# Optimization experiments

Hardware: AMD Instinct MI355X
Metric: run time of the kernel (lower is better)

Reference implementation:

```python
import jax, jax.numpy as jnp
import numpy as np

D_MODEL = 1024
N_HEADS = 16
DEPTH = D_MODEL // N_HEADS
D_FF = 4096
B, S = 2, 2048
EPS = 1e-5


def _layernorm(x, g, b):
    mu = jnp.mean(x, axis=-1, keepdims=True)
    var = jnp.mean(jnp.square(x - mu), axis=-1, keepdims=True)
    return (x - mu) * jax.lax.rsqrt(var + EPS) * g + b


def setup_inputs() -> dict:
    key = jax.random.key(0)
    ks = jax.random.split(key, 16)
    sd = 0.02
    d = {
        'x': jax.random.normal(ks[0], (B, S, D_MODEL), dtype=jnp.float32),
        'mask': jnp.ones((B, S), dtype=jnp.int32),
        'wq_w': jax.random.normal(ks[1], (D_MODEL, D_MODEL), dtype=jnp.float32) * sd,
        'wq_b': jnp.zeros((D_MODEL,), dtype=jnp.float32),
        'wk_w': jax.random.normal(ks[2], (D_MODEL, D_MODEL), dtype=jnp.float32) * sd,
        'wk_b': jnp.zeros((D_MODEL,), dtype=jnp.float32),
        'wv_w': jax.random.normal(ks[3], (D_MODEL, D_MODEL), dtype=jnp.float32) * sd,
        'wv_b': jnp.zeros((D_MODEL,), dtype=jnp.float32),
        'wo_w': jax.random.normal(ks[4], (D_MODEL, D_MODEL), dtype=jnp.float32) * sd,
        'wo_b': jnp.zeros((D_MODEL,), dtype=jnp.float32),
        'ffn_w1': jax.random.normal(ks[5], (D_MODEL, D_FF), dtype=jnp.float32) * sd,
        'ffn_b1': jnp.zeros((D_FF,), dtype=jnp.float32),
        'ffn_w2': jax.random.normal(ks[6], (D_FF, D_MODEL), dtype=jnp.float32) * sd,
        'ffn_b2': jnp.zeros((D_MODEL,), dtype=jnp.float32),
        'ln1_g': jnp.ones((D_MODEL,), dtype=jnp.float32),
        'ln1_b': jnp.zeros((D_MODEL,), dtype=jnp.float32),
        'ln2_g': jnp.ones((D_MODEL,), dtype=jnp.float32),
        'ln2_b': jnp.zeros((D_MODEL,), dtype=jnp.float32),
    }
    return d


def reference(x, mask, wq_w, wq_b, wk_w, wk_b, wv_w, wv_b, wo_w, wo_b,
              ffn_w1, ffn_b1, ffn_w2, ffn_b2, ln1_g, ln1_b, ln2_g, ln2_b):
    b, s, _ = x.shape
    # projections [B,S,D] -> [B,H,S,depth]
    def split_heads(t):
        return t.reshape(b, s, N_HEADS, DEPTH).transpose(0, 2, 1, 3)
    q = split_heads(x @ wq_w + wq_b)
    k = split_heads(x @ wk_w + wk_b)
    v = split_heads(x @ wv_w + wv_b)
    # scores [B,H,S,S]
    logits = jnp.einsum('bhqd,bhkd->bhqk', q, k) / jnp.sqrt(jnp.float32(DEPTH))
    m = mask[:, None, None, :]  # [B,1,1,S] broadcast over heads/query
    logits = jnp.where(m == 0, jnp.float32(-1e9), logits)
    attn = jax.nn.softmax(logits, axis=-1)
    ctx = jnp.einsum('bhqk,bhkd->bhqd', attn, v)
    ctx = ctx.transpose(0, 2, 1, 3).reshape(b, s, D_MODEL)
    attn_out = ctx @ wo_w + wo_b
    out1 = _layernorm(x + attn_out, ln1_g, ln1_b)
    ffn = jax.nn.relu(out1 @ ffn_w1 + ffn_b1) @ ffn_w2 + ffn_b2
    out2 = _layernorm(out1 + ffn, ln2_g, ln2_b)
    return out2
```

## Files before the change

### kernel.cpp

```cpp
#include <hip/hip_runtime.h>
#include <hip/hip_bf16.h>

#define D_MODEL 1024
#define N_HEADS 16
#define DEPTH   64
#define D_FF    4096
#define BATCH   2
#define SEQ     2048
#define NTOK    (BATCH * SEQ)
#define EPS     1e-5f

typedef __attribute__((ext_vector_type(8))) short short8;
typedef __attribute__((ext_vector_type(4))) float f32x4;
typedef __attribute__((ext_vector_type(4))) unsigned short ushort4v;
typedef __attribute__((ext_vector_type(8))) unsigned short ushort8v;

__device__ __forceinline__ unsigned short f2bf(float f) {
    union { __hip_bfloat16 h; unsigned short u; } cv;
    cv.h = __float2bfloat16(f);
    return cv.u;
}

__device__ __forceinline__ void gload16(const unsigned short* g, unsigned short* lds) {
    __builtin_amdgcn_global_load_lds(
        (const __attribute__((address_space(1))) void*)g,
        (__attribute__((address_space(3))) void*)lds, 16, 0, 0);
}

__global__ __launch_bounds__(256) void cast_bf16_kernel(
    const float* __restrict__ in, unsigned short* __restrict__ out, int n)
{
    int i = (blockIdx.x * 256 + threadIdx.x) * 8;
    if (i >= n) return;
    f32x4 a = *(const f32x4*)&in[i];
    f32x4 b = *(const f32x4*)&in[i + 4];
    ushort8v o;
    o[0] = f2bf(a[0]); o[1] = f2bf(a[1]); o[2] = f2bf(a[2]); o[3] = f2bf(a[3]);
    o[4] = f2bf(b[0]); o[5] = f2bf(b[1]); o[6] = f2bf(b[2]); o[7] = f2bf(b[3]);
    *(ushort8v*)&out[i] = o;
}

__global__ __launch_bounds__(256) void transpose_cast_kernel(
    const float* __restrict__ W, unsigned short* __restrict__ WT, int K, int N)
{
    __shared__ float t[64][65];
    const int bk = blockIdx.y * 64, bn = blockIdx.x * 64;
    const int c4 = threadIdx.x & 15, r0 = threadIdx.x >> 4;
#pragma unroll
    for (int i = 0; i < 4; ++i) {
        int k = r0 + i * 16;
        f32x4 v = *(const f32x4*)&W[(size_t)(bk + k) * N + bn + c4 * 4];
#pragma unroll
        for (int jj = 0; jj < 4; ++jj) t[k][c4 * 4 + jj] = v[jj];
    }
    __syncthreads();
#pragma unroll
    for (int i = 0; i < 4; ++i) {
        int n = r0 + i * 16;
        ushort4v o;
#pragma unroll
        for (int jj = 0; jj < 4; ++jj) o[jj] = f2bf(t[c4 * 4 + jj][n]);
        *(ushort4v*)&WT[(size_t)(bn + n) * K + bk + c4 * 4] = o;
    }
}

__global__ __launch_bounds__(256) void concat3_kernel(
    const float* __restrict__ a, const float* __restrict__ b,
    const float* __restrict__ c, float* __restrict__ o)
{
    int i = blockIdx.x * 256 + threadIdx.x;
    if (i < 1024) o[i] = a[i];
    else if (i < 2048) o[i] = b[i - 1024];
    else if (i < 3072) o[i] = c[i - 2048];
}

__global__ __launch_bounds__(256) void vtrans_kernel(
    const unsigned short* __restrict__ QKV, unsigned short* __restrict__ Vt)
{
    __shared__ unsigned short T[64][72];
    const int st = blockIdx.x * 64;
    const int h = blockIdx.y, b = blockIdx.z;
    const int tid = threadIdx.x;
    const size_t tok0 = (size_t)b * SEQ;
    const int LD = 3 * D_MODEL;
    const int r = tid >> 3, c8 = (tid & 7) * 8;
#pragma unroll
    for (int p = 0; p < 2; ++p) {
        int row = p * 32 + r;
        *(ushort8v*)&T[row][c8] =
            *(const ushort8v*)&QKV[(tok0 + st + row) * LD + 2048 + h * 64 + c8];
    }
    __syncthreads();
    const int bh = b * N_HEADS + h;
#pragma unroll
    for (int p = 0; p < 2; ++p) {
        int d = p * 32 + r;
        ushort8v o;
#pragma unroll
        for (int e = 0; e < 8; ++e) o[e] = T[c8 + e][d];
        *(ushort8v*)&Vt[((size_t)bh * 64 + d) * SEQ + st + c8] = o;
    }
}

__global__ __launch_bounds__(512, 2) void gemm256_kernel(
    const unsigned short* __restrict__ A, const unsigned short* __restrict__ BT,
    const float* __restrict__ bias, float* __restrict__ C,
    unsigned short* __restrict__ Cb,
    int M, int N, int lda, int kLen, int ksplit, int relu, int out_bf)
{
    __shared__ unsigned short As[2][256 * 64];
    __shared__ unsigned short Bs[2][256 * 64];
    const int tid = threadIdx.x;
    const int lane = tid & 63, w = tid >> 6;
    const int wr = w >> 2, wc = w & 3;
    const int lr = lane & 15, g = lane >> 4;

    const int nwg = gridDim.x;
    int wg = blockIdx.x;
    if ((nwg & 7) == 0) wg = (wg & 7) * (nwg >> 3) + (wg >> 3);
    if (ksplit > 1) {
        const int ntile = nwg / ksplit;
        const int split = wg / ntile;
        wg = wg % ntile;
        A  += (size_t)split * kLen;
        BT += (size_t)split * kLen;
        C  += (size_t)split * M * N;
    }
    const int gx = N >> 8;
    const int bm = (wg / gx) * 256, bn = (wg % gx) * 256;

    const int srow = (w << 3) + (lane >> 3);
    const int scol = ((lane & 7) ^ (lane >> 3)) << 3;
    const int ldst = (w << 9);

#define STG(P, Xs, bufi, hf, rb, k0)                                            \
    {                                                                            \
        gload16(P + (size_t)((rb) + (hf) * 128 + srow) * lda + (k0) + scol,      \
                &Xs[bufi][(hf) * 8192 + ldst]);                                  \
        gload16(P + (size_t)((rb) + (hf) * 128 + 64 + srow) * lda + (k0) + scol, \
                &Xs[bufi][(hf) * 8192 + 4096 + ldst]);                           \
    }

    const int NS = kLen >> 6;
    f32x4 acc[8][4] = {};

    STG(A,  As, 0, 0, bm, 0); STG(A,  As, 0, 1, bm, 0);
    STG(BT, Bs, 0, 0, bn, 0); STG(BT, Bs, 0, 1, bn, 0);
    if (NS > 1) { STG(BT, Bs, 1, 0, bn, 64); STG(BT, Bs, 1, 1, bn, 64); }
    asm volatile("s_waitcnt vmcnt(4)" ::: "memory");
    __builtin_amdgcn_s_barrier();
    asm volatile("" ::: "memory");

    int buf = 0;
    short8 af[4][2], b0[2][2], b1[2][2];
    for (int s = 0; s < NS; ++s) {
        const int kn1 = (s + 1) << 6, kn2 = (s + 2) << 6;

#pragma unroll
        for (int i = 0; i < 4; ++i)
#pragma unroll
            for (int kk = 0; kk < 2; ++kk)
                af[i][kk] = *(const short8*)&As[buf][(wr * 128 + i * 16 + lr) * 64
                                                    + (((kk * 4 + g) ^ (lr & 7)) << 3)];
#pragma unroll
        for (int j = 0; j < 2; ++j)
#pragma unroll
            for (int kk = 0; kk < 2; ++kk)
                b0[j][kk] = *(const short8*)&Bs[buf][(wc * 64 + j * 16 + lr) * 64
                                                    + (((kk * 4 + g) ^ (lr & 7)) << 3)];
        if (s + 1 < NS) STG(A, As, buf ^ 1, 0, bm, kn1);
        asm volatile("" ::: "memory");
        __builtin_amdgcn_s_barrier();
        asm volatile("" ::: "memory");
        __builtin_amdgcn_s_setprio(1);
#pragma unroll
        for (int i = 0; i < 4; ++i)
#pragma unroll
            for (int j = 0; j < 2; ++j) {
                acc[i][j] = __builtin_amdgcn_mfma_f32_16x16x32_bf16(af[i][0], b0[j][0], acc[i][j], 0, 0, 0);
                acc[i][j] = __builtin_amdgcn_mfma_f32_16x16x32_bf16(af[i][1], b0[j][1], acc[i][j], 0, 0, 0);
            }
        __builtin_amdgcn_s_setprio(0);
        asm volatile("" ::: "memory");
        __builtin_amdgcn_s_barrier();
        asm volatile("" ::: "memory");

#pragma unroll
        for (int j = 0; j < 2; ++j)
#pragma unroll
            for (int kk = 0; kk < 2; ++kk)
                b1[j][kk] = *(const short8*)&Bs[buf][(wc * 64 + (j + 2) * 16 + lr) * 64
                                                    + (((kk * 4 + g) ^ (lr & 7)) << 3)];
        if (s + 1 < NS) STG(A, As, buf ^ 1, 1, bm, kn1);
        asm volatile("" ::: "memory");
        __builtin_amdgcn_s_barrier();
        asm volatile("" ::: "memory");
        __builtin_amdgcn_s_setprio(1);
#pragma unroll
        for (int i = 0; i < 4; ++i)
#pragma unroll
            for (int j = 0; j < 2; ++j) {
                acc[i][j + 2] = __builtin_amdgcn_mfma_f32_16x16x32_bf16(af[i][0], b1[j][0], acc[i][j + 2], 0, 0, 0);
                acc[i][j + 2] = __builtin_amdgcn_mfma_f32_16x16x32_bf16(af[i][1], b1[j][1], acc[i][j + 2], 0, 0, 0);
            }
        __builtin_amdgcn_s_setprio(0);
        asm volatile("" ::: "memory");
        __builtin_amdgcn_s_barrier();
        asm volatile("" ::: "memory");

#pragma unroll
        for (int i = 0; i < 4; ++i)
#pragma unroll
            for (int kk = 0; kk < 2; ++kk)
                af[i][kk] = *(const short8*)&As[buf][(wr * 128 + 64 + i * 16 + lr) * 64
                                                    + (((kk * 4 + g) ^ (lr & 7)) << 3)];
        if (s + 2 < NS) STG(BT, Bs, buf, 0, bn, kn2);
        asm volatile("" ::: "memory");
        __builtin_amdgcn_s_barrier();
        asm volatile("" ::: "memory");
        __builtin_amdgcn_s_setprio(1);
#pragma unroll
        for (int i = 0; i < 4; ++i)
#pragma unroll
            for (int j = 0; j < 2; ++j) {
                acc[i + 4][j] = __builtin_amdgcn_mfma_f32_16x16x32_bf16(af[i][0], b0[j][0], acc[i + 4][j], 0, 0, 0);
                acc[i + 4][j] = __builtin_amdgcn_mfma_f32_16x16x32_bf16(af[i][1], b0[j][1], acc[i + 4][j], 0, 0, 0);
            }
        __builtin_amdgcn_s_setprio(0);
        asm volatile("" ::: "memory");
        __builtin_amdgcn_s_barrier();
        asm volatile("" ::: "memory");

        if (s + 2 < NS) STG(BT, Bs, buf, 1, bn, kn2);
        asm volatile("" ::: "memory");
        __builtin_amdgcn_s_barrier();
        asm volatile("" ::: "memory");
        __builtin_amdgcn_s_setprio(1);
#pragma unroll
        for (int i = 0; i < 4; ++i)
#pragma unroll
            for (int j = 0; j < 2; ++j) {
                acc[i + 4][j + 2] = __builtin_amdgcn_mfma_f32_16x16x32_bf16(af[i][0], b1[j][0], acc[i + 4][j + 2], 0, 0, 0);
                acc[i + 4][j + 2] = __builtin_amdgcn_mfma_f32_16x16x32_bf16(af[i][1], b1[j][1], acc[i + 4][j + 2], 0, 0, 0);
            }
        __builtin_amdgcn_s_setprio(0);
        asm volatile("s_waitcnt vmcnt(4)" ::: "memory");
        __builtin_amdgcn_s_barrier();
        asm volatile("" ::: "memory");

        buf ^= 1;
    }
#undef STG

#pragma unroll
    for (int i = 0; i < 8; ++i)
#pragma unroll
        for (int j = 0; j < 4; ++j) {
            const int col = bn + wc * 64 + j * 16 + lr;
            const float bv = bias ? bias[col] : 0.f;
#pragma unroll
            for (int r = 0; r < 4; ++r) {
                const int row = bm + wr * 128 + i * 16 + g * 4 + r;
                float v = acc[i][j][r] + bv;
                if (relu) v = fmaxf(v, 0.f);
                if (out_bf) Cb[(size_t)row * N + col] = f2bf(v);
                else        C [(size_t)row * N + col] = v;
            }
        }
}

__global__ __launch_bounds__(256) void gemm_bt_kernel(
    const unsigned short* __restrict__ A, const unsigned short* __restrict__ BT,
    const float* __restrict__ bias, float* __restrict__ C,
    unsigned short* __restrict__ Cb,
    int M, int N, int lda, int kLen, int relu, int out_bf)
{
    __shared__ unsigned short As[128 * 64];
    __shared__ unsigned short Bs[128 * 64];
    const int tid = threadIdx.x;
    const int lane = tid & 63, wv = tid >> 6;
    const int wr = wv >> 1, wc = wv & 1;
    const int bm = blockIdx.y * 128, bn = blockIdx.x * 128;
    const int kbase = blockIdx.z * kLen;
    const int lr = lane & 15, lk = (lane >> 4) << 3;

    C += (size_t)blockIdx.z * M * N;

    f32x4 acc[4][4] = {};

    for (int kt = 0; kt < kLen; kt += 64) {
#pragma unroll
        for (int c = 0; c < 4; ++c) {
            int e = c * 2048 + tid * 8;
            int row = e >> 6, k = e & 63;
            gload16(A  + (size_t)(bm + row) * lda + kbase + kt + k, As + c * 2048 + wv * 512);
            gload16(BT + (size_t)(bn + row) * lda + kbase + kt + k, Bs + c * 2048 + wv * 512);
        }
        __syncthreads();
#pragma unroll
        for (int kk = 0; kk < 2; ++kk) {
            short8 af[4], bfr[4];
#pragma unroll
            for (int i = 0; i < 4; ++i) {
                af[i]  = *(const short8*)&As[(wr * 64 + i * 16 + lr) * 64 + kk * 32 + lk];
                bfr[i] = *(const short8*)&Bs[(wc * 64 + i * 16 + lr) * 64 + kk * 32 + lk];
            }
#pragma unroll
            for (int i = 0; i < 4; ++i)
#pragma unroll
                for (int j = 0; j < 4; ++j)
                    acc[i][j] = __builtin_amdgcn_mfma_f32_16x16x32_bf16(
                        af[i], bfr[j], acc[i][j], 0, 0, 0);
        }
        __syncthreads();
    }

    const int r0 = bm + wr * 64, c0 = bn + wc * 64;
    const int rq = (lane >> 4) * 4;
#pragma unroll
    for (int i = 0; i < 4; ++i)
#pragma unroll
        for (int j = 0; j < 4; ++j) {
            int col = c0 + j * 16 + lr;
            float bv = bias ? bias[col] : 0.f;
#pragma unroll
            for (int r = 0; r < 4; ++r) {
                int row = r0 + i * 16 + rq + r;
                float v = acc[i][j][r] + bv;
                if (relu) v = fmaxf(v, 0.f);
                if (out_bf) Cb[(size_t)row * N + col] = f2bf(v);
                else        C [(size_t)row * N + col] = v;
            }
        }
}

__global__ __launch_bounds__(256, 2) void attn_mfma_kernel(
    const unsigned short* __restrict__ QKV,
    const unsigned short* __restrict__ Vt,
    const int* __restrict__ mask,
    unsigned short* __restrict__ ctx)
{
    const int tid = threadIdx.x;
    const int lane = tid & 63, w = tid >> 6;
    const int lr = lane & 15, g = lane >> 4;
    const int qt = blockIdx.x * 128;
    const int h = blockIdx.y, b = blockIdx.z;
    const int bh = b * N_HEADS + h;
    const size_t tok0 = (size_t)b * SEQ;
    const int LD = 3 * D_MODEL;

    __shared__ unsigned short Ks[2][64 * 64];
    __shared__ unsigned short Vs[2][64 * 64];
    __shared__ unsigned short Ps[4][32 * 64];
    __shared__ float Msk[2][64];

    short8 qf[2][2];
#pragma unroll
    for (int i = 0; i < 2; ++i)
#pragma unroll
        for (int kk = 0; kk < 2; ++kk)
            qf[i][kk] = *(const short8*)&QKV[(tok0 + qt + w * 32 + i * 16 + lr) * LD
                                             + h * 64 + kk * 32 + g * 8];

    const int rsub = w * 8 + (lane >> 3);
    const int slot = lane & 7;

    float m_[2] = {-1e30f, -1e30f}, l_[2] = {0.f, 0.f};
    f32x4 o_[2][4] = {};

    {
#pragma unroll
        for (int p = 0; p < 2; ++p) {
            const int row = p * 32 + rsub;
            const int ss = slot ^ (row & 7);
            gload16(QKV + (tok0 + row) * LD + D_MODEL + h * 64 + ss * 8,
                    &Ks[0][(p * 32 + w * 8) * 64]);
            gload16(Vt + ((size_t)bh * 64 + row) * SEQ + ss * 8,
                    &Vs[0][(p * 32 + w * 8) * 64]);
        }
        if (tid < 64) Msk[0][tid] = mask[b * SEQ + tid] ? 0.f : -1e9f;
    }
    __syncthreads();

    const int NT = SEQ / 64;
    int buf = 0;
    for (int t = 0; t < NT; ++t) {
        if (t + 1 < NT) {
            const int nb = buf ^ 1;
#pragma unroll
            for (int p = 0; p < 2; ++p) {
                const int row = p * 32 + rsub;
                const int ss = slot ^ (row & 7);
                gload16(QKV + (tok0 + (t + 1) * 64 + row) * LD + D_MODEL + h * 64 + ss * 8,
                        &Ks[nb][(p * 32 + w * 8) * 64]);
                gload16(Vt + ((size_t)bh * 64 + row) * SEQ + (t + 1) * 64 + ss * 8,
                        &Vs[nb][(p * 32 + w * 8) * 64]);
            }
            if (tid < 64) Msk[buf ^ 1][tid] = mask[b * SEQ + (t + 1) * 64 + tid] ? 0.f : -1e9f;
        }

        f32x4 sacc[2][4] = {};
#pragma unroll
        for (int j = 0; j < 4; ++j) {
            short8 kf0 = *(const short8*)&Ks[buf][(j * 16 + lr) * 64 + ((0 + g) ^ (lr & 7)) * 8];
            short8 kf1 = *(const short8*)&Ks[buf][(j * 16 + lr) * 64 + ((4 + g) ^ (lr & 7)) * 8];
#pragma unroll
            for (int i = 0; i < 2; ++i) {
                sacc[i][j] = __builtin_amdgcn_mfma_f32_16x16x32_bf16(kf0, qf[i][0], sacc[i][j], 0, 0, 0);
                sacc[i][j] = __builtin_amdgcn_mfma_f32_16x16x32_bf16(kf1, qf[i][1], sacc[i][j], 0, 0, 0);
            }
        }

        float mb[4][4];
#pragma unroll
        for (int j = 0; j < 4; ++j)
#pragma unroll
            for (int r = 0; r < 4; ++r) mb[j][r] = Msk[buf][j * 16 + g * 4 + r];

#pragma unroll
        for (int i = 0; i < 2; ++i) {
            float v[4][4];
            float tm = -1e30f;
#pragma unroll
            for (int j = 0; j < 4; ++j)
#pragma unroll
                for (int r = 0; r < 4; ++r) {
                    float x = sacc[i][j][r] * 0.125f + mb[j][r];
                    v[j][r] = x;
                    tm = fmaxf(tm, x);
                }
            tm = fmaxf(tm, __shfl_xor(tm, 16));
            tm = fmaxf(tm, __shfl_xor(tm, 32));
            const float nm = fmaxf(m_[i], tm);
            const float sc = __expf(m_[i] - nm);
            m_[i] = nm;
            float rs = 0.f;
#pragma unroll
            for (int j = 0; j < 4; ++j) {
                ushort4v pw;
#pragma unroll
                for (int r = 0; r < 4; ++r) {
                    float e = __expf(v[j][r] - nm);
                    rs += e;
                    pw[r] = f2bf(e);
                }
                *(ushort4v*)((char*)&Ps[w][0] + (i * 16 + lr) * 128
                             + ((j * 32 + g * 8) ^ ((lr & 7) << 4))) = pw;
            }
            rs += __shfl_xor(rs, 16);
            rs += __shfl_xor(rs, 32);
            l_[i] = l_[i] * sc + rs;
#pragma unroll
            for (int r = 0; r < 4; ++r) {
                float s_r = __shfl(sc, g * 4 + r);
#pragma unroll
                for (int dj = 0; dj < 4; ++dj) o_[i][dj][r] *= s_r;
            }
        }

#pragma unroll
        for (int kk = 0; kk < 2; ++kk) {
            short8 pf[2];
#pragma unroll
            for (int i = 0; i < 2; ++i)
                pf[i] = *(const short8*)&Ps[w][(i * 16 + lr) * 64 + ((kk * 4 + g) ^ (lr & 7)) * 8];
#pragma unroll
            for (int dj = 0; dj < 4; ++dj) {
                short8 vf = *(const short8*)&Vs[buf][(dj * 16 + lr) * 64 + ((kk * 4 + g) ^ (lr & 7)) * 8];
#pragma unroll
                for (int i = 0; i < 2; ++i)
                    o_[i][dj] = __builtin_amdgcn_mfma_f32_16x16x32_bf16(pf[i], vf, o_[i][dj], 0, 0, 0);
            }
        }

        __syncthreads();
        buf ^= 1;
    }

#pragma unroll
    for (int i = 0; i < 2; ++i) {
        const float invl = 1.f / l_[i];
#pragma unroll
        for (int r = 0; r < 4; ++r) {
            const float inv_r = __shfl(invl, g * 4 + r);
            const size_t tok = tok0 + qt + w * 32 + i * 16 + g * 4 + r;
#pragma unroll
            for (int dj = 0; dj < 4; ++dj)
                ctx[tok * D_MODEL + h * 64 + dj * 16 + lr] = f2bf(o_[i][dj][r] * inv_r);
        }
    }
}

__global__ __launch_bounds__(256) void reduce_ln_kernel(
    const float* __restrict__ P, int nsplit, const float* __restrict__ bias,
    const float* __restrict__ X, const float* __restrict__ g,
    const float* __restrict__ be, float* __restrict__ out,
    unsigned short* __restrict__ outb)
{
    const int row = blockIdx.x, tid = threadIdx.x;
    __shared__ float red[4];
    const size_t MN = (size_t)NTOK * D_MODEL;
    const size_t base = (size_t)row * D_MODEL + tid * 4;

    f32x4 s = *(const f32x4*)(X + base);
    f32x4 bb = *(const f32x4*)(bias + tid * 4);
    s += bb;
    for (int sp = 0; sp < nsplit; ++sp)
        s += *(const f32x4*)(P + sp * MN + base);

    float ls = s[0] + s[1] + s[2] + s[3];
#pragma unroll
    for (int o = 32; o > 0; o >>= 1) ls += __shfl_down(ls, o);
    if ((tid & 63) == 0) red[tid >> 6] = ls;
    __syncthreads();
    const float mu = (red[0] + red[1] + red[2] + red[3]) * (1.f / D_MODEL);
    __syncthreads();

    float d0 = s[0] - mu, d1 = s[1] - mu, d2 = s[2] - mu, d3 = s[3] - mu;
    float lv = d0 * d0 + d1 * d1 + d2 * d2 + d3 * d3;
#pragma unroll
    for (int o = 32; o > 0; o >>= 1) lv += __shfl_down(lv, o);
    if ((tid & 63) == 0) red[tid >> 6] = lv;
    __syncthreads();
    const float var = (red[0] + red[1] + red[2] + red[3]) * (1.f / D_MODEL);
    const float inv = rsqrtf(var + EPS);

    f32x4 gv = *(const f32x4*)(g + tid * 4);
    f32x4 bv = *(const f32x4*)(be + tid * 4);
    f32x4 o4 = {d0 * inv * gv[0] + bv[0], d1 * inv * gv[1] + bv[1],
                d2 * inv * gv[2] + bv[2], d3 * inv * gv[3] + bv[3]};
    *(f32x4*)(out + base) = o4;
    if (outb) {
        ushort4v ob = {f2bf(o4[0]), f2bf(o4[1]), f2bf(o4[2]), f2bf(o4[3])};
        *(ushort4v*)(outb + base) = ob;
    }
}

extern "C" void kernel_launch(void* const* d_in, const int* in_sizes, int n_in,
                              void* d_out, int out_size, void* d_ws, size_t ws_size,
                              hipStream_t stream) {
    const float* x      = (const float*)d_in[0];
    const int*   mask   = (const int*)  d_in[1];
    const float* wq_w   = (const float*)d_in[2];
    const float* wq_b   = (const float*)d_in[3];
    const float* wk_w   = (const float*)d_in[4];
    const float* wk_b   = (const float*)d_in[5];
    const float* wv_w   = (const float*)d_in[6];
    const float* wv_b   = (const float*)d_in[7];
    const float* wo_w   = (const float*)d_in[8];
    const float* wo_b   = (const float*)d_in[9];
    const float* ffn_w1 = (const float*)d_in[10];
    const float* ffn_b1 = (const float*)d_in[11];
    const float* ffn_w2 = (const float*)d_in[12];
    const float* ffn_b2 = (const float*)d_in[13];
    const float* ln1_g  = (const float*)d_in[14];
    const float* ln1_b  = (const float*)d_in[15];
    const float* ln2_g  = (const float*)d_in[16];
    const float* ln2_b  = (const float*)d_in[17];
    float* out = (float*)d_out;

    char* w = (char*)d_ws;
    const size_t MB = 1024 * 1024;
    unsigned short* actb    = (unsigned short*)(w);
    unsigned short* wqkvT   = (unsigned short*)(w + 8 * MB);
    float*          biasqkv = (float*)(w + 14 * MB);
    unsigned short* qkvb    = (unsigned short*)(w + 16 * MB);
    unsigned short* vt      = (unsigned short*)(w + 40 * MB);
    unsigned short* ctxb    = (unsigned short*)(w + 48 * MB);
    float*          woP     = (float*)(w);
    unsigned short* out1b   = (unsigned short*)(w + 40 * MB);
    unsigned short* fhb     = (unsigned short*)(w + 64 * MB);
    unsigned short* w2T     = (unsigned short*)(w + 96 * MB);
    unsigned short* woT     = (unsigned short*)(w + 104 * MB);
    float*          Out1    = (float*)(w + 104 * MB);
    unsigned short* w1T     = (unsigned short*)(w + 120 * MB);
    float*          f2P     = (float*)(w);

    dim3 blk(256);

    transpose_cast_kernel<<<dim3(16, 16), blk, 0, stream>>>(wq_w, wqkvT,               1024, 1024);
    transpose_cast_kernel<<<dim3(16, 16), blk, 0, stream>>>(wk_w, wqkvT + 1024 * 1024, 1024, 1024);
    transpose_cast_kernel<<<dim3(16, 16), blk, 0, stream>>>(wv_w, wqkvT + 2048 * 1024, 1024, 1024);
    transpose_cast_kernel<<<dim3(16, 16), blk, 0, stream>>>(wo_w, woT, 1024, 1024);
    transpose_cast_kernel<<<dim3(64, 16), blk, 0, stream>>>(ffn_w1, w1T, 1024, 4096);
    transpose_cast_kernel<<<dim3(16, 64), blk, 0, stream>>>(ffn_w2, w2T, 4096, 1024);
    concat3_kernel<<<dim3(12), blk, 0, stream>>>(wq_b, wk_b, wv_b, biasqkv);
    cast_bf16_kernel<<<dim3(2048), blk, 0, stream>>>(x, actb, NTOK * D_MODEL);

    gemm256_kernel<<<dim3(192), dim3(512), 0, stream>>>(actb, wqkvT, biasqkv, nullptr, qkvb,
                                                        NTOK, 3072, 1024, 1024, 1, 0, 1);
    vtrans_kernel<<<dim3(SEQ / 64, N_HEADS, BATCH), blk, 0, stream>>>(qkvb, vt);

    attn_mfma_kernel<<<dim3(SEQ / 128, N_HEADS, BATCH), blk, 0, stream>>>(qkvb, vt, mask, ctxb);

    gemm_bt_kernel<<<dim3(8, 32, 2), blk, 0, stream>>>(ctxb, woT, nullptr, woP, nullptr,
                                                       NTOK, 1024, 1024, 512, 0, 0);
    reduce_ln_kernel<<<dim3(NTOK), blk, 0, stream>>>(woP, 2, wo_b, x, ln1_g, ln1_b,
                                                     Out1, out1b);
    gemm256_kernel<<<dim3(256), dim3(512), 0, stream>>>(out1b, w1T, ffn_b1, nullptr, fhb,
                                                        NTOK, D_FF, 1024, 1024, 1, 1, 1);
    gemm256_kernel<<<dim3(256), dim3(512), 0, stream>>>(fhb, w2T, nullptr, f2P, nullptr,
                                                        NTOK, 1024, 4096, 1024, 4, 0, 0);
    reduce_ln_kernel<<<dim3(NTOK), blk, 0, stream>>>(f2P, 4, ffn_b2, Out1, ln2_g, ln2_b,
                                                     out, nullptr);
}
```

Measured before the change: 278.1 us.

## Shrink attention query tile, use exp2 softmax with lazy rescaling

The attention kernel now processes 64 query rows per block, 16 per wave, instead of 128. This doubles the grid, and the launch bound is raised to 3 blocks per SM to improve occupancy and reduce register pressure. The softmax folds the 1/sqrt(d) scale and log2(e) into a single FMA and uses a raw v_exp_f32 instruction. It also skips rescaling the running max and output unless the new max exceeds the old by more than 8, cutting per-tile exp and multiply work. The trade-off is that K/V tiles are reloaded for twice as many blocks, raising global and LDS traffic per unit of compute, and each wave has less MFMA work to hide latency.

```diff
diff --git a/kernel.cpp b/kernel.cpp
--- a/kernel.cpp
+++ b/kernel.cpp
@@ -19,6 +19,12 @@
     union { __hip_bfloat16 h; unsigned short u; } cv;
     cv.h = __float2bfloat16(f);
     return cv.u;
+}
+
+__device__ __forceinline__ float exp2_fast(float x) {
+    float r;
+    asm("v_exp_f32 %0, %1" : "=v"(r) : "v"(x));
+    return r;
 }
 
 __device__ __forceinline__ void gload16(const unsigned short* g, unsigned short* lds) {
@@ -334,7 +340,7 @@
         }
 }
 
-__global__ __launch_bounds__(256, 2) void attn_mfma_kernel(
+__global__ __launch_bounds__(256, 3) void attn_mfma_kernel(
     const unsigned short* __restrict__ QKV,
     const unsigned short* __restrict__ Vt,
     const int* __restrict__ mask,
@@ -343,30 +349,29 @@
     const int tid = threadIdx.x;
     const int lane = tid & 63, w = tid >> 6;
     const int lr = lane & 15, g = lane >> 4;
-    const int qt = blockIdx.x * 128;
+    const int qt = blockIdx.x * 64;
     const int h = blockIdx.y, b = blockIdx.z;
     const int bh = b * N_HEADS + h;
     const size_t tok0 = (size_t)b * SEQ;
     const int LD = 3 * D_MODEL;
+    const float C1 = 0.18033688f;
 
     __shared__ unsigned short Ks[2][64 * 64];
     __shared__ unsigned short Vs[2][64 * 64];
-    __shared__ unsigned short Ps[4][32 * 64];
+    __shared__ unsigned short Ps[4][16 * 64];
     __shared__ float Msk[2][64];
 
-    short8 qf[2][2];
-#pragma unroll
-    for (int i = 0; i < 2; ++i)
-#pragma unroll
-        for (int kk = 0; kk < 2; ++kk)
-            qf[i][kk] = *(const short8*)&QKV[(tok0 + qt + w * 32 + i * 16 + lr) * LD
-                                             + h * 64 + kk * 32 + g * 8];
+    short8 qf[2];
+#pragma unroll
+    for (int kk = 0; kk < 2; ++kk)
+        qf[kk] = *(const short8*)&QKV[(tok0 + qt + w * 16 + lr) * LD
+                                      + h * 64 + kk * 32 + g * 8];
 
     const int rsub = w * 8 + (lane >> 3);
     const int slot = lane & 7;
 
-    float m_[2] = {-1e30f, -1e30f}, l_[2] = {0.f, 0.f};
-    f32x4 o_[2][4] = {};
+    float m_ = -1e30f, l_ = 0.f;
+    f32x4 o_[4] = {};
 
     {
 #pragma unroll
@@ -399,77 +404,66 @@
             if (tid < 64) Msk[buf ^ 1][tid] = mask[b * SEQ + (t + 1) * 64 + tid] ? 0.f : -1e9f;
         }
 
-        f32x4 sacc[2][4] = {};
+        f32x4 sacc[4] = {};
 #pragma unroll
         for (int j = 0; j < 4; ++j) {
             short8 kf0 = *(const short8*)&Ks[buf][(j * 16 + lr) * 64 + ((0 + g) ^ (lr & 7)) * 8];
             short8 kf1 = *(const short8*)&Ks[buf][(j * 16 + lr) * 64 + ((4 + g) ^ (lr & 7)) * 8];
-#pragma unroll
-            for (int i = 0; i < 2; ++i) {
-                sacc[i][j] = __builtin_amdgcn_mfma_f32_16x16x32_bf16(kf0, qf[i][0], sacc[i][j], 0, 0, 0);
-                sacc[i][j] = __builtin_amdgcn_mfma_f32_16x16x32_bf16(kf1, qf[i][1], sacc[i][j], 0, 0, 0);
-            }
-        }
-
-        float mb[4][4];
-#pragma unroll
-        for (int j = 0; j < 4; ++j)
-#pragma unroll
-            for (int r = 0; r < 4; ++r) mb[j][r] = Msk[buf][j * 16 + g * 4 + r];
-
-#pragma unroll
-        for (int i = 0; i < 2; ++i) {
-            float v[4][4];
-            float tm = -1e30f;
-#pragma unroll
-            for (int j = 0; j < 4; ++j)
-#pragma unroll
-                for (int r = 0; r < 4; ++r) {
-                    float x = sacc[i][j][r] * 0.125f + mb[j][r];
-                    v[j][r] = x;
-                    tm = fmaxf(tm, x);
-                }
-            tm = fmaxf(tm, __shfl_xor(tm, 16));
-            tm = fmaxf(tm, __shfl_xor(tm, 32));
-            const float nm = fmaxf(m_[i], tm);
-            const float sc = __expf(m_[i] - nm);
-            m_[i] = nm;
-            float rs = 0.f;
-#pragma unroll
-            for (int j = 0; j < 4; ++j) {
-                ushort4v pw;
-#pragma unroll
-                for (int r = 0; r < 4; ++r) {
-                    float e = __expf(v[j][r] - nm);
-                    rs += e;
-                    pw[r] = f2bf(e);
-                }
-                *(ushort4v*)((char*)&Ps[w][0] + (i * 16 + lr) * 128
-                             + ((j * 32 + g * 8) ^ ((lr & 7) << 4))) = pw;
-            }
-            rs += __shfl_xor(rs, 16);
-            rs += __shfl_xor(rs, 32);
-            l_[i] = l_[i] * sc + rs;
+            sacc[j] = __builtin_amdgcn_mfma_f32_16x16x32_bf16(kf0, qf[0], sacc[j], 0, 0, 0);
+            sacc[j] = __builtin_amdgcn_mfma_f32_16x16x32_bf16(kf1, qf[1], sacc[j], 0, 0, 0);
+        }
+
+        float x[4][4];
+        float mj[4];
+#pragma unroll
+        for (int j = 0; j < 4; ++j) {
+            f32x4 mrow = *(const f32x4*)&Msk[buf][j * 16 + g * 4];
+#pragma unroll
+            for (int r = 0; r < 4; ++r)
+                x[j][r] = fmaf(sacc[j][r], C1, mrow[r]);
+            mj[j] = fmaxf(fmaxf(x[j][0], x[j][1]), fmaxf(x[j][2], x[j][3]));
+        }
+        float tm = fmaxf(fmaxf(mj[0], mj[1]), fmaxf(mj[2], mj[3]));
+        tm = fmaxf(tm, __shfl_xor(tm, 16));
+        tm = fmaxf(tm, __shfl_xor(tm, 32));
+
+        if (__any(tm > m_ + 8.f)) {
+            const float nm = fmaxf(m_, tm);
+            const float sc = exp2_fast(m_ - nm);
+            m_ = nm;
+            l_ *= sc;
 #pragma unroll
             for (int r = 0; r < 4; ++r) {
-                float s_r = __shfl(sc, g * 4 + r);
-#pragma unroll
-                for (int dj = 0; dj < 4; ++dj) o_[i][dj][r] *= s_r;
-            }
-        }
+                const float s_r = __shfl(sc, g * 4 + r);
+#pragma unroll
+                for (int dj = 0; dj < 4; ++dj) o_[dj][r] *= s_r;
+            }
+        }
+
+        float rs = 0.f;
+#pragma unroll
+        for (int j = 0; j < 4; ++j) {
+            ushort4v pw;
+#pragma unroll
+            for (int r = 0; r < 4; ++r) {
+                const float e = exp2_fast(x[j][r] - m_);
+                rs += e;
+                pw[r] = f2bf(e);
+            }
+            *(ushort4v*)((char*)&Ps[w][0] + lr * 128
+                         + ((j * 32 + g * 8) ^ ((lr & 7) << 4))) = pw;
+        }
+        rs += __shfl_xor(rs, 16);
+        rs += __shfl_xor(rs, 32);
+        l_ += rs;
 
 #pragma unroll
         for (int kk = 0; kk < 2; ++kk) {
-            short8 pf[2];
-#pragma unroll
-            for (int i = 0; i < 2; ++i)
-                pf[i] = *(const short8*)&Ps[w][(i * 16 + lr) * 64 + ((kk * 4 + g) ^ (lr & 7)) * 8];
+            short8 pf = *(const short8*)&Ps[w][lr * 64 + ((kk * 4 + g) ^ (lr & 7)) * 8];
 #pragma unroll
             for (int dj = 0; dj < 4; ++dj) {
                 short8 vf = *(const short8*)&Vs[buf][(dj * 16 + lr) * 64 + ((kk * 4 + g) ^ (lr & 7)) * 8];
-#pragma unroll
-                for (int i = 0; i < 2; ++i)
-                    o_[i][dj] = __builtin_amdgcn_mfma_f32_16x16x32_bf16(pf[i], vf, o_[i][dj], 0, 0, 0);
+                o_[dj] = __builtin_amdgcn_mfma_f32_16x16x32_bf16(pf, vf, o_[dj], 0, 0, 0);
             }
         }
 
@@ -477,17 +471,14 @@
         buf ^= 1;
     }
 
-#pragma unroll
-    for (int i = 0; i < 2; ++i) {
-        const float invl = 1.f / l_[i];
-#pragma unroll
-        for (int r = 0; r < 4; ++r) {
-            const float inv_r = __shfl(invl, g * 4 + r);
-            const size_t tok = tok0 + qt + w * 32 + i * 16 + g * 4 + r;
-#pragma unroll
-            for (int dj = 0; dj < 4; ++dj)
-                ctx[tok * D_MODEL + h * 64 + dj * 16 + lr] = f2bf(o_[i][dj][r] * inv_r);
-        }
+    const float invl = 1.f / l_;
+#pragma unroll
+    for (int r = 0; r < 4; ++r) {
+        const float inv_r = __shfl(invl, g * 4 + r);
+        const size_t tok = tok0 + qt + w * 16 + g * 4 + r;
+#pragma unroll
+        for (int dj = 0; dj < 4; ++dj)
+            ctx[tok * D_MODEL + h * 64 + dj * 16 + lr] = f2bf(o_[dj][r] * inv_r);
     }
 }
 
@@ -591,7 +582,7 @@
                                                         NTOK, 3072, 1024, 1024, 1, 0, 1);
     vtrans_kernel<<<dim3(SEQ / 64, N_HEADS, BATCH), blk, 0, stream>>>(qkvb, vt);
 
-    attn_mfma_kernel<<<dim3(SEQ / 128, N_HEADS, BATCH), blk, 0, stream>>>(qkvb, vt, mask, ctxb);
+    attn_mfma_kernel<<<dim3(SEQ / 64, N_HEADS, BATCH), blk, 0, stream>>>(qkvb, vt, mask, ctxb);
 
     gemm_bt_kernel<<<dim3(8, 32, 2), blk, 0, stream>>>(ctxb, woT, nullptr, woP, nullptr,
                                                        NTOK, 1024, 1024, 512, 0, 0);
```

New measurement: 292.1 us. 5.0% more time.

## Split attention KV range in two with merge kernel, exp2 softmax with lazy rescale

Applied to the files above, without the earlier changes.

Attention now splits each head's key/value sequence into two halves handled by separate blocks (split-KV). Partial unnormalized outputs plus max and sum are written to fp32 workspace, and a new merge kernel combines them into the bf16 context. Softmax switches to a raw v_exp_f32 base-2 exponent with the log2e factor folded into the scale. It also skips the running-max rescale unless the max grows by more than 8, and raises launch bounds to 3 blocks per CU. The aim is more blocks for occupancy (the old grid was only 512 blocks) and fewer ALU ops per tile, at the cost of extra fp32 traffic and one extra launch.

```diff
diff --git a/kernel.cpp b/kernel.cpp
--- a/kernel.cpp
+++ b/kernel.cpp
@@ -19,6 +19,12 @@
     union { __hip_bfloat16 h; unsigned short u; } cv;
     cv.h = __float2bfloat16(f);
     return cv.u;
+}
+
+__device__ __forceinline__ float exp2_fast(float x) {
+    float r;
+    asm("v_exp_f32 %0, %1" : "=v"(r) : "v"(x));
+    return r;
 }
 
 __device__ __forceinline__ void gload16(const unsigned short* g, unsigned short* lds) {
@@ -334,20 +340,23 @@
         }
 }
 
-__global__ __launch_bounds__(256, 2) void attn_mfma_kernel(
+__global__ __launch_bounds__(256, 3) void attn_mfma_kernel(
     const unsigned short* __restrict__ QKV,
     const unsigned short* __restrict__ Vt,
     const int* __restrict__ mask,
-    unsigned short* __restrict__ ctx)
+    float* __restrict__ Op, float* __restrict__ ml)
 {
     const int tid = threadIdx.x;
     const int lane = tid & 63, w = tid >> 6;
     const int lr = lane & 15, g = lane >> 4;
     const int qt = blockIdx.x * 128;
-    const int h = blockIdx.y, b = blockIdx.z;
+    const int h = blockIdx.y;
+    const int b = blockIdx.z >> 1, sp = blockIdx.z & 1;
     const int bh = b * N_HEADS + h;
     const size_t tok0 = (size_t)b * SEQ;
+    const int kvb0 = sp * (SEQ / 2);
     const int LD = 3 * D_MODEL;
+    const float C1 = 0.18033688f;
 
     __shared__ unsigned short Ks[2][64 * 64];
     __shared__ unsigned short Vs[2][64 * 64];
@@ -373,30 +382,31 @@
         for (int p = 0; p < 2; ++p) {
             const int row = p * 32 + rsub;
             const int ss = slot ^ (row & 7);
-            gload16(QKV + (tok0 + row) * LD + D_MODEL + h * 64 + ss * 8,
+            gload16(QKV + (tok0 + kvb0 + row) * LD + D_MODEL + h * 64 + ss * 8,
                     &Ks[0][(p * 32 + w * 8) * 64]);
-            gload16(Vt + ((size_t)bh * 64 + row) * SEQ + ss * 8,
+            gload16(Vt + ((size_t)bh * 64 + row) * SEQ + kvb0 + ss * 8,
                     &Vs[0][(p * 32 + w * 8) * 64]);
         }
-        if (tid < 64) Msk[0][tid] = mask[b * SEQ + tid] ? 0.f : -1e9f;
+        if (tid < 64) Msk[0][tid] = mask[b * SEQ + kvb0 + tid] ? 0.f : -1e9f;
     }
     __syncthreads();
 
-    const int NT = SEQ / 64;
+    const int NT = (SEQ / 2) / 64;
     int buf = 0;
     for (int t = 0; t < NT; ++t) {
         if (t + 1 < NT) {
             const int nb = buf ^ 1;
+            const int kvn = kvb0 + (t + 1) * 64;
 #pragma unroll
             for (int p = 0; p < 2; ++p) {
                 const int row = p * 32 + rsub;
                 const int ss = slot ^ (row & 7);
-                gload16(QKV + (tok0 + (t + 1) * 64 + row) * LD + D_MODEL + h * 64 + ss * 8,
+                gload16(QKV + (tok0 + kvn + row) * LD + D_MODEL + h * 64 + ss * 8,
                         &Ks[nb][(p * 32 + w * 8) * 64]);
-                gload16(Vt + ((size_t)bh * 64 + row) * SEQ + (t + 1) * 64 + ss * 8,
+                gload16(Vt + ((size_t)bh * 64 + row) * SEQ + kvn + ss * 8,
                         &Vs[nb][(p * 32 + w * 8) * 64]);
             }
-            if (tid < 64) Msk[buf ^ 1][tid] = mask[b * SEQ + (t + 1) * 64 + tid] ? 0.f : -1e9f;
+            if (tid < 64) Msk[nb][tid] = mask[b * SEQ + kvn + tid] ? 0.f : -1e9f;
         }
 
         f32x4 sacc[2][4] = {};
@@ -413,34 +423,44 @@
 
         float mb[4][4];
 #pragma unroll
-        for (int j = 0; j < 4; ++j)
-#pragma unroll
-            for (int r = 0; r < 4; ++r) mb[j][r] = Msk[buf][j * 16 + g * 4 + r];
+        for (int j = 0; j < 4; ++j) {
+            f32x4 mrow = *(const f32x4*)&Msk[buf][j * 16 + g * 4];
+#pragma unroll
+            for (int r = 0; r < 4; ++r) mb[j][r] = mrow[r];
+        }
 
 #pragma unroll
         for (int i = 0; i < 2; ++i) {
-            float v[4][4];
+            float x[4][4];
             float tm = -1e30f;
 #pragma unroll
             for (int j = 0; j < 4; ++j)
 #pragma unroll
                 for (int r = 0; r < 4; ++r) {
-                    float x = sacc[i][j][r] * 0.125f + mb[j][r];
-                    v[j][r] = x;
-                    tm = fmaxf(tm, x);
+                    x[j][r] = fmaf(sacc[i][j][r], C1, mb[j][r]);
+                    tm = fmaxf(tm, x[j][r]);
                 }
             tm = fmaxf(tm, __shfl_xor(tm, 16));
             tm = fmaxf(tm, __shfl_xor(tm, 32));
-            const float nm = fmaxf(m_[i], tm);
-            const float sc = __expf(m_[i] - nm);
-            m_[i] = nm;
+            if (__any(tm > m_[i] + 8.f)) {
+                const float nm = fmaxf(m_[i], tm);
+                const float sc = exp2_fast(m_[i] - nm);
+                m_[i] = nm;
+                l_[i] *= sc;
+#pragma unroll
+                for (int r = 0; r < 4; ++r) {
+                    const float s_r = __shfl(sc, g * 4 + r);
+#pragma unroll
+                    for (int dj = 0; dj < 4; ++dj) o_[i][dj][r] *= s_r;
+                }
+            }
             float rs = 0.f;
 #pragma unroll
             for (int j = 0; j < 4; ++j) {
                 ushort4v pw;
 #pragma unroll
                 for (int r = 0; r < 4; ++r) {
-                    float e = __expf(v[j][r] - nm);
+                    const float e = exp2_fast(x[j][r] - m_[i]);
                     rs += e;
                     pw[r] = f2bf(e);
                 }
@@ -449,13 +469,7 @@
             }
             rs += __shfl_xor(rs, 16);
             rs += __shfl_xor(rs, 32);
-            l_[i] = l_[i] * sc + rs;
-#pragma unroll
-            for (int r = 0; r < 4; ++r) {
-                float s_r = __shfl(sc, g * 4 + r);
-#pragma unroll
-                for (int dj = 0; dj < 4; ++dj) o_[i][dj][r] *= s_r;
-            }
+            l_[i] += rs;
         }
 
 #pragma unroll
@@ -477,18 +491,45 @@
         buf ^= 1;
     }
 
+    const int rowbase = (sp * 32 + bh) * 2048;
 #pragma unroll
     for (int i = 0; i < 2; ++i) {
-        const float invl = 1.f / l_[i];
 #pragma unroll
         for (int r = 0; r < 4; ++r) {
-            const float inv_r = __shfl(invl, g * 4 + r);
-            const size_t tok = tok0 + qt + w * 32 + i * 16 + g * 4 + r;
-#pragma unroll
-            for (int dj = 0; dj < 4; ++dj)
-                ctx[tok * D_MODEL + h * 64 + dj * 16 + lr] = f2bf(o_[i][dj][r] * inv_r);
-        }
-    }
+            const int q = qt + w * 32 + i * 16 + g * 4 + r;
+            float* op = Op + (size_t)(rowbase + q) * 64;
+#pragma unroll
+            for (int dj = 0; dj < 4; ++dj) op[dj * 16 + lr] = o_[i][dj][r];
+        }
+        if (g == 0) {
+            const int q2 = qt + w * 32 + i * 16 + lr;
+            float2 v; v.x = m_[i]; v.y = l_[i];
+            ((float2*)ml)[rowbase + q2] = v;
+        }
+    }
+}
+
+__global__ __launch_bounds__(256) void attn_merge_kernel(
+    const float* __restrict__ Op, const float* __restrict__ ml,
+    unsigned short* __restrict__ ctx)
+{
+    const int tid = threadIdx.x;
+    const int row = blockIdx.x * 16 + (tid >> 4);
+    const int d4 = (tid & 15) * 4;
+    const int bh = row >> 11, q = row & 2047;
+    const int b = bh >> 4, h = bh & 15;
+    const float2 v0 = ((const float2*)ml)[row];
+    const float2 v1 = ((const float2*)ml)[65536 + row];
+    const float m = fmaxf(v0.x, v1.x);
+    const float a0 = exp2_fast(v0.x - m), a1 = exp2_fast(v1.x - m);
+    const float inv = 1.f / (v0.y * a0 + v1.y * a1);
+    f32x4 O0 = *(const f32x4*)&Op[(size_t)row * 64 + d4];
+    f32x4 O1 = *(const f32x4*)&Op[((size_t)65536 + row) * 64 + d4];
+    ushort4v o;
+#pragma unroll
+    for (int e = 0; e < 4; ++e)
+        o[e] = f2bf((O0[e] * a0 + O1[e] * a1) * inv);
+    *(ushort4v*)&ctx[((size_t)(b * SEQ + q)) * D_MODEL + h * 64 + d4] = o;
 }
 
 __global__ __launch_bounds__(256) void reduce_ln_kernel(
@@ -567,6 +608,8 @@
     unsigned short* qkvb    = (unsigned short*)(w + 16 * MB);
     unsigned short* vt      = (unsigned short*)(w + 40 * MB);
     unsigned short* ctxb    = (unsigned short*)(w + 48 * MB);
+    float*          Opb     = (float*)(w + 56 * MB);
+    float*          mlb     = (float*)(w + 88 * MB);
     float*          woP     = (float*)(w);
     unsigned short* out1b   = (unsigned short*)(w + 40 * MB);
     unsigned short* fhb     = (unsigned short*)(w + 64 * MB);
@@ -591,7 +634,9 @@
                                                         NTOK, 3072, 1024, 1024, 1, 0, 1);
     vtrans_kernel<<<dim3(SEQ / 64, N_HEADS, BATCH), blk, 0, stream>>>(qkvb, vt);
 
-    attn_mfma_kernel<<<dim3(SEQ / 128, N_HEADS, BATCH), blk, 0, stream>>>(qkvb, vt, mask, ctxb);
+    attn_mfma_kernel<<<dim3(SEQ / 128, N_HEADS, BATCH * 2), blk, 0, stream>>>(qkvb, vt, mask,
+                                                                              Opb, mlb);
+    attn_merge_kernel<<<dim3((BATCH * N_HEADS * SEQ) / 16), blk, 0, stream>>>(Opb, mlb, ctxb);
 
     gemm_bt_kernel<<<dim3(8, 32, 2), blk, 0, stream>>>(ctxb, woT, nullptr, woP, nullptr,
                                                        NTOK, 1024, 1024, 512, 0, 0);
```

Measured after the change: 277.7 us. No clear change (-0.1%).
